# Kernel tuning notes

Measured on AMD Instinct MI355X. Metric: run time of the kernel, lower is better.

## Reference

```python
import jax, jax.numpy as jnp
import numpy as np

N, E, DIN, D, H, L = 4096, 65536, 128, 256, 4, 3
DH = D // H


def _ln(x, g, b, eps=1e-5):
    m = jnp.mean(x, axis=-1, keepdims=True)
    v = jnp.mean((x - m) ** 2, axis=-1, keepdims=True)
    return (x - m) * jax.lax.rsqrt(v + eps) * g + b


def _gcn(x, w, b, row, col, n):
    # PyG GCNConv: add self-loops, symmetric normalization D^-1/2 A D^-1/2, aggregate at col (target)
    ar = jnp.arange(n, dtype=row.dtype)
    r = jnp.concatenate([row, ar])
    c = jnp.concatenate([col, ar])
    deg = jax.ops.segment_sum(jnp.ones(r.shape[0], x.dtype), c, num_segments=n)
    dinv = jnp.where(deg > 0, deg ** -0.5, 0.0)
    norm = dinv[r] * dinv[c]  # (E+N,)
    msg = x @ w.T  # (N, out)
    return jax.ops.segment_sum(norm[:, None] * msg[r], c, num_segments=n) + b


def setup_inputs() -> dict:
    key = jax.random.key(0)
    ks = jax.random.split(key, 12)
    rnd = lambda i, shape: jax.random.normal(ks[i], shape, jnp.float32) * 0.05
    return {
        "node_features": jax.random.normal(ks[0], (N, DIN), jnp.float32),
        "edge_index": jax.random.randint(ks[1], (2, E), 0, N, jnp.int32),
        "gcn1_w": rnd(2, (D, DIN)), "gcn1_b": jnp.zeros((D,), jnp.float32),
        "gcn2_w": rnd(3, (D, D)), "gcn2_b": jnp.zeros((D,), jnp.float32),
        "edge_w": rnd(4, (H, 3)), "edge_b": jnp.zeros((H,), jnp.float32),
        "proj_w": rnd(5, (D, DIN + D)), "proj_b": jnp.zeros((D,), jnp.float32),
        "wqkv": rnd(6, (L, 3 * D, D)), "bqkv": jnp.zeros((L, 3 * D), jnp.float32),
        "wo": rnd(7, (L, D, D)), "bo": jnp.zeros((L, D), jnp.float32),
        "ffn_w1": rnd(8, (L, 4 * D, D)), "ffn_b1": jnp.zeros((L, 4 * D), jnp.float32),
        "ffn_w2": rnd(9, (L, D, 4 * D)), "ffn_b2": jnp.zeros((L, D), jnp.float32),
        "ln1_g": jnp.ones((L, D), jnp.float32), "ln1_b": jnp.zeros((L, D), jnp.float32),
        "ln2_g": jnp.ones((L, D), jnp.float32), "ln2_b": jnp.zeros((L, D), jnp.float32),
        "out_w": rnd(10, (1, D)), "out_b": jnp.zeros((1,), jnp.float32),
    }


def reference(node_features, edge_index, gcn1_w, gcn1_b, gcn2_w, gcn2_b,
              edge_w, edge_b, proj_w, proj_b, wqkv, bqkv, wo, bo,
              ffn_w1, ffn_b1, ffn_w2, ffn_b2, ln1_g, ln1_b, ln2_g, ln2_b,
              out_w, out_b):
    n = node_features.shape[0]
    row, col = edge_index[0], edge_index[1]
    # two-layer GCN
    h = jax.nn.relu(_gcn(node_features, gcn1_w, gcn1_b, row, col, n))
    g = _gcn(h, gcn2_w, gcn2_b, row, col, n)
    x = jnp.concatenate([node_features, g], axis=-1) @ proj_w.T + proj_b  # (N, D)
    # edge-aware attention bias: per-edge linear+sigmoid scattered into dense (H, N, N)
    feat = jnp.stack([row.astype(x.dtype), col.astype(x.dtype),
                      jnp.ones(row.shape[0], x.dtype)], axis=-1)  # (E, 3)
    bpe = jax.nn.sigmoid(feat @ edge_w.T + edge_b)  # (E, H)
    bias = jnp.zeros((H, n, n), x.dtype).at[:, row, col].set(bpe.T)
    scale = 1.0 / np.sqrt(DH)
    for l in range(L):
        qkv = x @ wqkv[l].T + bqkv[l]
        q, k, v = jnp.split(qkv, 3, axis=-1)
        q = q.reshape(n, H, DH); k = k.reshape(n, H, DH); v = v.reshape(n, H, DH)
        s = jnp.einsum('nhd,mhd->hnm', q, k) * scale + bias
        a = jax.nn.softmax(s, axis=-1)
        o = jnp.einsum('hnm,mhd->nhd', a, v).reshape(n, D) @ wo[l].T + bo[l]
        x = _ln(x + o, ln1_g[l], ln1_b[l])
        f = jax.nn.relu(x @ ffn_w1[l].T + ffn_b1[l]) @ ffn_w2[l].T + ffn_b2[l]
        x = _ln(x + f, ln2_g[l], ln2_b[l])
    return jax.nn.sigmoid(x @ out_w.T + out_b)  # (N, 1) probs
```

## Files before the change

kernel.cpp:

```cpp
#include <hip/hip_runtime.h>
#include <math.h>

#define NN 4096
#define NE 65536
#define DIN 128
#define DM 256
#define NH 4
#define NL 3
#define NCH 4
#define TPC (NN / 64 / NCH)
#define NBKT 16384

typedef __attribute__((ext_vector_type(8))) short bf16x8;
typedef __attribute__((ext_vector_type(4))) float f32x4;

__device__ inline ushort f2b(float f) {
    union { float f; uint u; } v; v.f = f;
    uint r = v.u + 0x7fffu + ((v.u >> 16) & 1u);
    return (ushort)(r >> 16);
}

__device__ inline uint cvt_pk_bf16(float lo, float hi) {
    uint r;
    asm("v_cvt_pk_bf16_f32 %0, %1, %2" : "=v"(r) : "v"(lo), "v"(hi));
    return r;
}

__device__ inline void gl_lds16(const ushort* g, ushort* l) {
    __builtin_amdgcn_global_load_lds(
        (const __attribute__((address_space(1))) void*)g,
        (__attribute__((address_space(3))) void*)l, 16, 0, 0);
}


__global__ void k_edge1(const int* __restrict__ row, const int* __restrict__ col,
                        uint* __restrict__ bitmap, int* __restrict__ cnt_c,
                        int* __restrict__ bcnt, unsigned char* __restrict__ flag) {
    int e = blockIdx.x * 256 + threadIdx.x;
    if (e >= NE) return;
    int r = row[e], c = col[e];
    atomicAdd(&cnt_c[c], 1);
    uint idx = (uint)r * 4096u + (uint)c;
    uint m = 1u << (idx & 31);
    uint old = atomicOr(&bitmap[idx >> 5], m);
    int isnew = (old & m) ? 0 : 1;
    flag[e] = (unsigned char)isnew;
    if (isnew) atomicAdd(&bcnt[(r >> 4) * 64 + (c >> 6)], 1);
}

__global__ void k_edge2(const int* __restrict__ row, const int* __restrict__ col,
                        const unsigned char* __restrict__ flag,
                        const int* __restrict__ sc, int* __restrict__ fc, int* __restrict__ csc_row,
                        const int* __restrict__ bstart, int* __restrict__ bfill,
                        ushort* __restrict__ ents) {
    int e = blockIdx.x * 256 + threadIdx.x;
    if (e >= NE) return;
    int r = row[e], c = col[e];
    csc_row[sc[c] + atomicAdd(&fc[c], 1)] = r;
    if (flag[e]) {
        int key = (r >> 4) * 64 + (c >> 6);
        ents[bstart[key] + atomicAdd(&bfill[key], 1)] = (ushort)(((r & 15) << 6) | (c & 63));
    }
}

template <int N>
__global__ void k_scan(const int* __restrict__ cnt, int* __restrict__ start) {
    __shared__ int part[256];
    const int C = N / 256;
    int t = threadIdx.x;
    int s = 0;
    for (int i = 0; i < C; ++i) s += cnt[t * C + i];
    part[t] = s;
    __syncthreads();
    if (t == 0) {
        int acc = 0;
        for (int i = 0; i < 256; ++i) { int v = part[i]; part[i] = acc; acc += v; }
        start[N] = acc;
    }
    __syncthreads();
    int acc = part[t];
    for (int i = 0; i < C; ++i) { start[t * C + i] = acc; acc += cnt[t * C + i]; }
}

__global__ void k_dinv(const int* __restrict__ cnt_c, float* __restrict__ dinv) {
    int i = blockIdx.x * 256 + threadIdx.x;
    if (i < NN) dinv[i] = 1.0f / sqrtf((float)(cnt_c[i] + 1));
}

struct CvtP { const float* s[8]; ushort* d[8]; int n[8]; };
__global__ void k_cvt(CvtP p) {
    int y = blockIdx.y;
    int base = (blockIdx.x * 256 + threadIdx.x) * 4;
    if (base >= p.n[y]) return;
    float4 v = *(const float4*)(p.s[y] + base);
    float sc = 1.f;
    if (y == 1 && ((base >> 8) % 768) < 256) sc = 0.125f;
    ushort4 o;
    o.x = f2b(v.x * sc); o.y = f2b(v.y * sc); o.z = f2b(v.z * sc); o.w = f2b(v.w * sc);
    *(ushort4*)(p.d[y] + base) = o;
}

__global__ void k_scaleb(const float* __restrict__ b, float* __restrict__ o) {
    int i = blockIdx.x * 256 + threadIdx.x;
    if (i < NL * 768) o[i] = b[i] * (((i % 768) < 256) ? 0.125f : 1.f);
}

template <int FLAGS>
__global__ __launch_bounds__(256) void k_gemm_b(
    const ushort* __restrict__ A, int lda,
    const ushort* __restrict__ B, int ldb,
    float* __restrict__ Cf, ushort* __restrict__ Cb, ushort* __restrict__ Cb2, int ldc,
    int K, const float* __restrict__ bias) {
    __shared__ ushort As[128 * 64];
    __shared__ ushort Bs[128 * 64];
    const int tid = threadIdx.x;
    const int w = tid >> 6, l = tid & 63;
    const int l15 = l & 15, l4 = l >> 4;
    const int row0 = blockIdx.y * 128, col0 = blockIdx.x * 128;
    const int wm = (w >> 1) * 64, wn = (w & 1) * 64;
    f32x4 acc[4][4];
#pragma unroll
    for (int i = 0; i < 4; ++i)
#pragma unroll
        for (int j = 0; j < 4; ++j) acc[i][j] = (f32x4){0.f, 0.f, 0.f, 0.f};
    for (int k0 = 0; k0 < K; k0 += 64) {
#pragma unroll
        for (int i = 0; i < 4; ++i) {
            int ci = tid + 256 * i;
            int r = ci >> 3, s = ci & 7;
            bf16x8 va = *(const bf16x8*)(A + (long)(row0 + r) * lda + k0 + s * 8);
            *(bf16x8*)&As[r * 64 + ((s ^ (r & 7)) * 8)] = va;
            bf16x8 vb = *(const bf16x8*)(B + (long)(col0 + r) * ldb + k0 + s * 8);
            *(bf16x8*)&Bs[r * 64 + ((s ^ (r & 7)) * 8)] = vb;
        }
        __syncthreads();
#pragma unroll
        for (int kk = 0; kk < 2; ++kk) {
            bf16x8 af[4], bfr[4];
#pragma unroll
            for (int i = 0; i < 4; ++i) {
                int ar = wm + i * 16 + l15;
                af[i] = *(const bf16x8*)&As[ar * 64 + (((kk * 4 + l4) ^ (ar & 7)) * 8)];
                int br = wn + i * 16 + l15;
                bfr[i] = *(const bf16x8*)&Bs[br * 64 + (((kk * 4 + l4) ^ (br & 7)) * 8)];
            }
#pragma unroll
            for (int i = 0; i < 4; ++i)
#pragma unroll
                for (int j = 0; j < 4; ++j)
                    acc[i][j] = __builtin_amdgcn_mfma_f32_16x16x32_bf16(af[i], bfr[j], acc[i][j], 0, 0, 0);
        }
        __syncthreads();
    }
#pragma unroll
    for (int i = 0; i < 4; ++i)
#pragma unroll
        for (int j = 0; j < 4; ++j) {
            int rb = row0 + wm + i * 16;
            int cb = col0 + wn + j * 16 + l15;
            float bv = bias ? bias[cb] : 0.f;
            if (FLAGS & 16) {
                if (cb < 512) {
#pragma unroll
                    for (int q = 0; q < 4; ++q)
                        Cb[(long)(rb + l4 * 4 + q) * 512 + cb] = f2b(acc[i][j][q] + bv);
                } else {
                    ushort4 o4;
                    o4.x = f2b(acc[i][j][0] + bv);
                    o4.y = f2b(acc[i][j][1] + bv);
                    o4.z = f2b(acc[i][j][2] + bv);
                    o4.w = f2b(acc[i][j][3] + bv);
                    *(ushort4*)(Cb2 + (long)(cb - 512) * NN + rb + l4 * 4) = o4;
                }
            } else if (FLAGS & 8) {
                ushort4 o4;
                o4.x = f2b(acc[i][j][0] + bv);
                o4.y = f2b(acc[i][j][1] + bv);
                o4.z = f2b(acc[i][j][2] + bv);
                o4.w = f2b(acc[i][j][3] + bv);
                *(ushort4*)(Cb + (long)cb * ldc + rb + l4 * 4) = o4;
            } else {
#pragma unroll
                for (int q = 0; q < 4; ++q) {
                    int r = rb + l4 * 4 + q;
                    float v = acc[i][j][q] + bv;
                    if (FLAGS & 4) v = fmaxf(v, 0.f);
                    if (FLAGS & 1) Cf[(long)r * ldc + cb] = v;
                    if (FLAGS & 2) Cb[(long)r * ldc + cb] = f2b(v);
                }
            }
        }
}

__global__ __launch_bounds__(256) void k_gemm_ln(
    const ushort* __restrict__ A, int lda,
    const ushort* __restrict__ B, int ldb, int K,
    const float* __restrict__ bias,
    float* __restrict__ x, ushort* __restrict__ xb,
    const float* __restrict__ gam, const float* __restrict__ bet) {
    __shared__ ushort As[16 * 64];
    __shared__ ushort Bs[256 * 64];
    __shared__ float red[4][16][2];
    const int tid = threadIdx.x;
    const int w = tid >> 6, l = tid & 63;
    const int l15 = l & 15, l4 = l >> 4;
    const int row0 = blockIdx.x * 16;
    f32x4 acc[4];
#pragma unroll
    for (int j = 0; j < 4; ++j) acc[j] = (f32x4){0.f, 0.f, 0.f, 0.f};
    for (int k0 = 0; k0 < K; k0 += 64) {
        if (tid < 128) {
            int r = tid >> 3, s = tid & 7;
            bf16x8 va = *(const bf16x8*)(A + (long)(row0 + r) * lda + k0 + s * 8);
            *(bf16x8*)&As[r * 64 + ((s ^ (r & 7)) * 8)] = va;
        }
#pragma unroll
        for (int i = 0; i < 8; ++i) {
            int idx = i * 256 + tid;
            int r = idx >> 3, s = idx & 7;
            bf16x8 vb = *(const bf16x8*)(B + (long)r * ldb + k0 + s * 8);
            *(bf16x8*)&Bs[r * 64 + ((s ^ (r & 7)) * 8)] = vb;
        }
        __syncthreads();
#pragma unroll
        for (int kk = 0; kk < 2; ++kk) {
            bf16x8 af = *(const bf16x8*)&As[l15 * 64 + (((kk * 4 + l4) ^ (l15 & 7)) * 8)];
#pragma unroll
            for (int j = 0; j < 4; ++j) {
                int br = w * 64 + j * 16 + l15;
                bf16x8 bfr = *(const bf16x8*)&Bs[br * 64 + (((kk * 4 + l4) ^ (br & 7)) * 8)];
                acc[j] = __builtin_amdgcn_mfma_f32_16x16x32_bf16(af, bfr, acc[j], 0, 0, 0);
            }
        }
        __syncthreads();
    }
    float val[4][4];
#pragma unroll
    for (int j = 0; j < 4; ++j) {
        int c = w * 64 + j * 16 + l15;
        float bv = bias[c];
#pragma unroll
        for (int q = 0; q < 4; ++q) {
            int r = row0 + l4 * 4 + q;
            val[j][q] = acc[j][q] + bv + x[(long)r * DM + c];
        }
    }
    float sum[4], sq[4];
#pragma unroll
    for (int q = 0; q < 4; ++q) {
        sum[q] = (val[0][q] + val[1][q]) + (val[2][q] + val[3][q]);
        sq[q] = (val[0][q] * val[0][q] + val[1][q] * val[1][q]) +
                (val[2][q] * val[2][q] + val[3][q] * val[3][q]);
    }
#pragma unroll
    for (int o = 1; o < 16; o <<= 1)
#pragma unroll
        for (int q = 0; q < 4; ++q) {
            sum[q] += __shfl_xor(sum[q], o);
            sq[q] += __shfl_xor(sq[q], o);
        }
    if (l15 == 0)
#pragma unroll
        for (int q = 0; q < 4; ++q) {
            red[w][l4 * 4 + q][0] = sum[q];
            red[w][l4 * 4 + q][1] = sq[q];
        }
    __syncthreads();
    float mean[4], rs[4];
#pragma unroll
    for (int q = 0; q < 4; ++q) {
        int rl = l4 * 4 + q;
        float ts = (red[0][rl][0] + red[1][rl][0]) + (red[2][rl][0] + red[3][rl][0]);
        float tq = (red[0][rl][1] + red[1][rl][1]) + (red[2][rl][1] + red[3][rl][1]);
        float m = ts * (1.f / 256.f);
        float var = tq * (1.f / 256.f) - m * m;
        mean[q] = m;
        rs[q] = rsqrtf(var + 1e-5f);
    }
#pragma unroll
    for (int j = 0; j < 4; ++j) {
        int c = w * 64 + j * 16 + l15;
        float gv = gam[c], bv = bet[c];
#pragma unroll
        for (int q = 0; q < 4; ++q) {
            int r = row0 + l4 * 4 + q;
            float ov = (val[j][q] - mean[q]) * rs[q] * gv + bv;
            x[(long)r * DM + c] = ov;
            xb[(long)r * DM + c] = f2b(ov);
        }
    }
}

template <int ACT, int B16>
__global__ void k_gcn_agg(const float* __restrict__ msg, const int* __restrict__ sc,
                          const int* __restrict__ csc_row, const float* __restrict__ dinv,
                          const float* __restrict__ bias,
                          float* __restrict__ outf, ushort* __restrict__ outb) {
    int j = blockIdx.x;
    int d = threadIdx.x;
    float acc = 0.f;
    int a = sc[j], b = sc[j + 1];
    for (int i = a; i < b; ++i) {
        int r = csc_row[i];
        acc += dinv[r] * msg[(long)r * DM + d];
    }
    float dj = dinv[j];
    float v = dj * acc + dj * dj * msg[(long)j * DM + d] + bias[d];
    if (ACT) v = fmaxf(v, 0.f);
    if (B16) outb[(long)j * DM + d] = f2b(v);
    else outf[(long)j * DM + d] = v;
}

__global__ void k_concat(const ushort* __restrict__ nfb, const float* __restrict__ g,
                         ushort* __restrict__ xcb) {
    long i = (long)blockIdx.x * 256 + threadIdx.x;
    if (i >= (long)NN * 384) return;
    int r = (int)(i / 384), c = (int)(i % 384);
    xcb[i] = (c < DIN) ? nfb[(long)r * DIN + c] : f2b(g[(long)r * DM + (c - DIN)]);
}

__global__ __launch_bounds__(256, 4) void k_attn(
    const ushort* __restrict__ qkb, const ushort* __restrict__ vT,
    const float* __restrict__ ew, const float* __restrict__ eb,
    const int* __restrict__ bstart, const ushort* __restrict__ ents,
    float* __restrict__ opart, float2* __restrict__ ml) {
    __shared__ ushort Klds[2][4096];
    __shared__ ushort Vlds[2][4096];
    __shared__ ushort Pl[4096];
    const int qb = blockIdx.x, h = blockIdx.y, cz = blockIdx.z;
    const int tid = threadIdx.x, w = tid >> 6, l = tid & 63;
    const int l15 = l & 15, l4 = l >> 4;
    const float w0 = ew[h * 3 + 0], w1 = ew[h * 3 + 1], w2 = ew[h * 3 + 2] + eb[h];
    bf16x8 qf[2];
    {
        const ushort* qp = qkb + (long)(qb * 64 + w * 16 + l15) * 512 + h * 64 + l4 * 8;
        qf[0] = *(const bf16x8*)(qp);
        qf[1] = *(const bf16x8*)(qp + 32);
    }
    const ushort* Kb = qkb + 256 + h * 64;
    const ushort* Vb = vT + (long)(h * 64) * NN;
    f32x4 o[4];
#pragma unroll
    for (int f = 0; f < 4; ++f) o[f] = (f32x4){0.f, 0.f, 0.f, 0.f};
    float m_run = -1e30f, l_run = 0.f;
    char* P = (char*)&Pl[w * 1024];
    const int bktW = (qb * 4 + w) * 64;
    const int t0 = cz * TPC;

    auto stage = [&](int b, int t) {
#pragma unroll
        for (int i = 0; i < 2; ++i) {
            int idx = i * 256 + w * 64 + l;
            int r = idx >> 3, sl = idx & 7;
            gl_lds16(Kb + (long)(t * 64 + r) * 512 + ((sl ^ (r & 7)) * 8),
                     &Klds[b][(i * 256 + w * 64) * 8]);
            gl_lds16(Vb + (long)r * NN + t * 64 + ((sl ^ (r & 7)) * 8),
                     &Vlds[b][(i * 256 + w * 64) * 8]);
        }
    };

    int bs_c = bstart[bktW + t0], be_c = bstart[bktW + t0 + 1];
    stage(0, t0);
    int cur = 0;
    for (int tt = 0; tt < TPC; ++tt) {
        const int t = t0 + tt;
        asm volatile("s_waitcnt lgkmcnt(0)" ::: "memory");
        __builtin_amdgcn_s_barrier();
        int bs_n = 0, be_n = 0;
        if (tt + 1 < TPC) {
            stage(cur ^ 1, t + 1);
            bs_n = bstart[bktW + t + 1];
            be_n = bstart[bktW + t + 2];
            asm volatile("s_waitcnt vmcnt(4)" ::: "memory");
        } else {
            asm volatile("s_waitcnt vmcnt(0)" ::: "memory");
        }
        __builtin_amdgcn_sched_barrier(0);
        __builtin_amdgcn_s_barrier();
        __builtin_amdgcn_sched_barrier(0);

        const ushort* Kl = Klds[cur];
        const ushort* Vl = Vlds[cur];
        f32x4 s4[4];
#pragma unroll
        for (int f = 0; f < 4; ++f) {
            int kc = f * 16 + l15;
            bf16x8 k0 = *(const bf16x8*)&Kl[kc * 64 + ((l4 ^ (kc & 7)) * 8)];
            bf16x8 k1 = *(const bf16x8*)&Kl[kc * 64 + (((4 + l4) ^ (kc & 7)) * 8)];
            f32x4 a = (f32x4){0.f, 0.f, 0.f, 0.f};
            a = __builtin_amdgcn_mfma_f32_16x16x32_bf16(k0, qf[0], a, 0, 0, 0);
            a = __builtin_amdgcn_mfma_f32_16x16x32_bf16(k1, qf[1], a, 0, 0, 0);
            s4[f] = a;
        }
        for (int i = bs_c; i < be_c; ++i) {
            int rc = (int)ents[i];
            int r4 = rc >> 6, c6 = rc & 63;
            if (l15 == r4 && ((c6 >> 2) & 3) == l4) {
                float arg = w0 * (float)(qb * 64 + w * 16 + r4) + w1 * (float)(t * 64 + c6) + w2;
                float sig = 1.f / (1.f + __expf(-arg));
                switch (((c6 >> 4) << 2) | (c6 & 3)) {
                    case 0:  s4[0][0] += sig; break; case 1:  s4[0][1] += sig; break;
                    case 2:  s4[0][2] += sig; break; case 3:  s4[0][3] += sig; break;
                    case 4:  s4[1][0] += sig; break; case 5:  s4[1][1] += sig; break;
                    case 6:  s4[1][2] += sig; break; case 7:  s4[1][3] += sig; break;
                    case 8:  s4[2][0] += sig; break; case 9:  s4[2][1] += sig; break;
                    case 10: s4[2][2] += sig; break; case 11: s4[2][3] += sig; break;
                    case 12: s4[3][0] += sig; break; case 13: s4[3][1] += sig; break;
                    case 14: s4[3][2] += sig; break; case 15: s4[3][3] += sig; break;
                }
            }
        }
        float ma = fmaxf(fmaxf(s4[0][0], s4[0][1]), fmaxf(s4[0][2], s4[0][3]));
        float mb = fmaxf(fmaxf(s4[1][0], s4[1][1]), fmaxf(s4[1][2], s4[1][3]));
        float mc = fmaxf(fmaxf(s4[2][0], s4[2][1]), fmaxf(s4[2][2], s4[2][3]));
        float md = fmaxf(fmaxf(s4[3][0], s4[3][1]), fmaxf(s4[3][2], s4[3][3]));
        float me = fmaxf(fmaxf(ma, mb), fmaxf(mc, md));
        me = fmaxf(me, __shfl_xor(me, 16));
        me = fmaxf(me, __shfl_xor(me, 32));
        if (!__all(me <= m_run + 8.f)) {
            float mn = fmaxf(m_run, me);
            float fac = __expf(m_run - mn);
            m_run = mn;
            l_run *= fac;
#pragma unroll
            for (int f = 0; f < 4; ++f)
#pragma unroll
                for (int r = 0; r < 4; ++r) o[f][r] *= fac;
        }
        float rp[4];
#pragma unroll
        for (int f = 0; f < 4; ++f) {
            float p0 = __expf(s4[f][0] - m_run);
            float p1 = __expf(s4[f][1] - m_run);
            float p2 = __expf(s4[f][2] - m_run);
            float p3 = __expf(s4[f][3] - m_run);
            s4[f][0] = p0; s4[f][1] = p1; s4[f][2] = p2; s4[f][3] = p3;
            rp[f] = (p0 + p1) + (p2 + p3);
        }
        float rsum = (rp[0] + rp[1]) + (rp[2] + rp[3]);
        rsum += __shfl_xor(rsum, 16);
        rsum += __shfl_xor(rsum, 32);
        l_run += rsum;
#pragma unroll
        for (int f = 0; f < 4; ++f)
#pragma unroll
            for (int p = 0; p < 2; ++p) {
                uint u = cvt_pk_bf16(s4[f][2 * p], s4[f][2 * p + 1]);
                int slot = f * 2 + (l4 >> 1);
                int byte = l15 * 128 + ((slot ^ (l15 & 7)) << 4) + (l4 & 1) * 8 + p * 4;
                *(uint*)(P + byte) = u;
            }
        asm volatile("s_waitcnt lgkmcnt(0)" ::: "memory");
        __builtin_amdgcn_sched_barrier(0);
#pragma unroll
        for (int ks = 0; ks < 2; ++ks) {
            bf16x8 pb = *(const bf16x8*)(P + l15 * 128 + (((ks * 4 + l4) ^ (l15 & 7)) << 4));
#pragma unroll
            for (int fd = 0; fd < 4; ++fd) {
                int d = fd * 16 + l15;
                bf16x8 vfr = *(const bf16x8*)&Vl[d * 64 + (((ks * 4 + l4) ^ (d & 7)) * 8)];
                o[fd] = __builtin_amdgcn_mfma_f32_16x16x32_bf16(vfr, pb, o[fd], 0, 0, 0);
            }
        }
        bs_c = bs_n; be_c = be_n;
        cur ^= 1;
    }
    long base = (((long)cz * NH + h) * NN + qb * 64 + w * 16 + l15) * 64;
#pragma unroll
    for (int fd = 0; fd < 4; ++fd)
#pragma unroll
        for (int r = 0; r < 4; ++r)
            opart[base + fd * 16 + l4 * 4 + r] = o[fd][r];
    if (l4 == 0)
        ml[((long)cz * NH + h) * NN + qb * 64 + w * 16 + l15] = make_float2(m_run, l_run);
}

__global__ __launch_bounds__(256) void k_comb(const float* __restrict__ opart,
                                              const float2* __restrict__ ml,
                                              ushort* __restrict__ attnOb) {
    int t = blockIdx.x * 256 + threadIdx.x;
    int d = t & 63;
    int r = (t >> 6) & (NN - 1);
    int h = t >> 18;
    float2 mls[NCH];
    float M = -1e30f;
#pragma unroll
    for (int c = 0; c < NCH; ++c) {
        mls[c] = ml[((long)c * NH + h) * NN + r];
        M = fmaxf(M, mls[c].x);
    }
    float s = 0.f, ov = 0.f;
#pragma unroll
    for (int c = 0; c < NCH; ++c) {
        float e = __expf(mls[c].x - M);
        s += mls[c].y * e;
        ov += opart[(((long)c * NH + h) * NN + r) * 64 + d] * e;
    }
    attnOb[(long)r * DM + h * 64 + d] = f2b(ov / s);
}


__global__ void k_out(const float* __restrict__ x, const float* __restrict__ w,
                      const float* __restrict__ b, float* __restrict__ out) {
    int row = blockIdx.x;
    int lane = threadIdx.x;
    float s = 0.f;
#pragma unroll
    for (int i = 0; i < 4; ++i) s += x[(long)row * DM + lane + 64 * i] * w[lane + 64 * i];
#pragma unroll
    for (int o = 1; o < 64; o <<= 1) s += __shfl_xor(s, o);
    if (lane == 0) out[row] = 1.f / (1.f + expf(-(s + b[0])));
}

__global__ void k_sentinel(float* out, int n) {
    int i = blockIdx.x * 256 + threadIdx.x;
    if (i < n) out[i] = 1.0e9f;
}


extern "C" void kernel_launch(void* const* d_in, const int* in_sizes, int n_in,
                              void* d_out, int out_size, void* d_ws, size_t ws_size,
                              hipStream_t stream) {
    const float* nf = (const float*)d_in[0];
    const int* ei = (const int*)d_in[1];
    const int* erow = ei;
    const int* ecol = ei + NE;
    const float* gcn1_w = (const float*)d_in[2];
    const float* gcn1_b = (const float*)d_in[3];
    const float* gcn2_w = (const float*)d_in[4];
    const float* gcn2_b = (const float*)d_in[5];
    const float* edge_w = (const float*)d_in[6];
    const float* edge_b = (const float*)d_in[7];
    const float* proj_w = (const float*)d_in[8];
    const float* proj_b = (const float*)d_in[9];
    const float* wqkv = (const float*)d_in[10];
    const float* bqkv = (const float*)d_in[11];
    const float* wo = (const float*)d_in[12];
    const float* bo = (const float*)d_in[13];
    const float* ffn_w1 = (const float*)d_in[14];
    const float* ffn_b1 = (const float*)d_in[15];
    const float* ffn_w2 = (const float*)d_in[16];
    const float* ffn_b2 = (const float*)d_in[17];
    const float* ln1_g = (const float*)d_in[18];
    const float* ln1_b = (const float*)d_in[19];
    const float* ln2_g = (const float*)d_in[20];
    const float* ln2_b = (const float*)d_in[21];
    const float* out_w = (const float*)d_in[22];
    const float* out_b = (const float*)d_in[23];
    float* out = (float*)d_out;

    char* wp = (char*)d_ws;
    size_t off = 0;
    auto alloc = [&](size_t bytes) -> void* {
        void* p = wp + off;
        off = (off + bytes + 255) & ~(size_t)255;
        return p;
    };
    char* big = (char*)alloc((size_t)NCH * NH * NN * 64 * 4);
    float* msg = (float*)big;
    float* opart = (float*)big;
    ushort* ffnHb = (ushort*)big;
    float* x = (float*)alloc((size_t)NN * DM * 4);
    ushort* xb = (ushort*)alloc((size_t)NN * DM * 2);
    ushort* xcb = (ushort*)alloc((size_t)NN * 384 * 2);
    ushort* hb = (ushort*)alloc((size_t)NN * DM * 2);
    float* g = (float*)alloc((size_t)NN * DM * 4);
    ushort* qkb = (ushort*)alloc((size_t)NN * 512 * 2);
    ushort* vT = (ushort*)alloc((size_t)DM * NN * 2);
    ushort* attnOb = (ushort*)alloc((size_t)NN * DM * 2);
    float2* ml = (float2*)alloc((size_t)NCH * NH * NN * 8);
    ushort* nfb = (ushort*)alloc((size_t)NN * DIN * 2);
    ushort* wqkvb = (ushort*)alloc((size_t)NL * 768 * DM * 2);
    ushort* wob = (ushort*)alloc((size_t)NL * DM * DM * 2);
    ushort* f1b = (ushort*)alloc((size_t)NL * 1024 * DM * 2);
    ushort* f2bw = (ushort*)alloc((size_t)NL * DM * 1024 * 2);
    ushort* g1b = (ushort*)alloc((size_t)DM * DIN * 2);
    ushort* g2b = (ushort*)alloc((size_t)DM * DM * 2);
    ushort* pjb = (ushort*)alloc((size_t)DM * 384 * 2);
    float* bq2 = (float*)alloc((size_t)NL * 768 * 4);
    uint* bitmap = (uint*)alloc((size_t)NN * NN / 8);
    unsigned char* flag = (unsigned char*)alloc(NE);
    int* cnt_c = (int*)alloc((size_t)NN * 4);
    int* bcnt = (int*)alloc((size_t)NBKT * 4);
    int* sc = (int*)alloc((size_t)(NN + 1) * 4);
    int* bstart = (int*)alloc((size_t)(NBKT + 1) * 4);
    int* fc = (int*)alloc((size_t)NN * 4);
    int* bfill = (int*)alloc((size_t)NBKT * 4);
    int* csc_row = (int*)alloc((size_t)NE * 4);
    ushort* ents = (ushort*)alloc((size_t)NE * 2);
    float* dinv = (float*)alloc((size_t)NN * 4);

    if (off > ws_size) {
        k_sentinel<<<(out_size + 255) / 256, 256, 0, stream>>>(out, out_size);
        return;
    }

    hipMemsetAsync(bitmap, 0, (size_t)NN * NN / 8, stream);
    hipMemsetAsync(cnt_c, 0, NN * 4, stream);
    hipMemsetAsync(bcnt, 0, NBKT * 4, stream);
    hipMemsetAsync(fc, 0, NN * 4, stream);
    hipMemsetAsync(bfill, 0, NBKT * 4, stream);
    k_edge1<<<NE / 256, 256, 0, stream>>>(erow, ecol, bitmap, cnt_c, bcnt, flag);
    k_scan<NN><<<1, 256, 0, stream>>>(cnt_c, sc);
    k_scan<NBKT><<<1, 256, 0, stream>>>(bcnt, bstart);
    k_edge2<<<NE / 256, 256, 0, stream>>>(erow, ecol, flag, sc, fc, csc_row, bstart, bfill, ents);
    k_dinv<<<NN / 256, 256, 0, stream>>>(cnt_c, dinv);

    CvtP cp;
    cp.s[0] = nf;      cp.d[0] = nfb;   cp.n[0] = NN * DIN;
    cp.s[1] = wqkv;    cp.d[1] = wqkvb; cp.n[1] = NL * 768 * DM;
    cp.s[2] = wo;      cp.d[2] = wob;   cp.n[2] = NL * DM * DM;
    cp.s[3] = ffn_w1;  cp.d[3] = f1b;   cp.n[3] = NL * 1024 * DM;
    cp.s[4] = ffn_w2;  cp.d[4] = f2bw;  cp.n[4] = NL * DM * 1024;
    cp.s[5] = gcn1_w;  cp.d[5] = g1b;   cp.n[5] = DM * DIN;
    cp.s[6] = gcn2_w;  cp.d[6] = g2b;   cp.n[6] = DM * DM;
    cp.s[7] = proj_w;  cp.d[7] = pjb;   cp.n[7] = DM * 384;
    k_cvt<<<dim3(768, 8), 256, 0, stream>>>(cp);
    k_scaleb<<<(NL * 768 + 255) / 256, 256, 0, stream>>>(bqkv, bq2);

    k_gemm_b<1><<<dim3(DM / 128, NN / 128), 256, 0, stream>>>(
        nfb, DIN, g1b, DIN, msg, nullptr, nullptr, DM, DIN, nullptr);
    k_gcn_agg<1, 1><<<NN, DM, 0, stream>>>(msg, sc, csc_row, dinv, gcn1_b, nullptr, hb);
    k_gemm_b<1><<<dim3(DM / 128, NN / 128), 256, 0, stream>>>(
        hb, DM, g2b, DM, msg, nullptr, nullptr, DM, DM, nullptr);
    k_gcn_agg<0, 0><<<NN, DM, 0, stream>>>(msg, sc, csc_row, dinv, gcn2_b, g, nullptr);
    k_concat<<<(NN * 384 + 255) / 256, 256, 0, stream>>>(nfb, g, xcb);
    k_gemm_b<3><<<dim3(DM / 128, NN / 128), 256, 0, stream>>>(
        xcb, 384, pjb, 384, x, xb, nullptr, DM, 384, proj_b);

    for (int l = 0; l < NL; ++l) {
        k_gemm_b<18><<<dim3(768 / 128, NN / 128), 256, 0, stream>>>(
            xb, DM, wqkvb + (long)l * 768 * DM, DM, nullptr, qkb, vT, 512, DM,
            bq2 + (long)l * 768);
        k_attn<<<dim3(NN / 64, NH, NCH), 256, 0, stream>>>(
            qkb, vT, edge_w, edge_b, bstart, ents, opart, ml);
        k_comb<<<NN * NH * 64 / 256, 256, 0, stream>>>(opart, ml, attnOb);
        k_gemm_ln<<<NN / 16, 256, 0, stream>>>(
            attnOb, DM, wob + (long)l * DM * DM, DM, DM, bo + (long)l * DM,
            x, xb, ln1_g + (long)l * DM, ln1_b + (long)l * DM);
        k_gemm_b<6><<<dim3(1024 / 128, NN / 128), 256, 0, stream>>>(
            xb, DM, f1b + (long)l * 1024 * DM, DM, nullptr, ffnHb, nullptr, 1024, DM,
            ffn_b1 + (long)l * 1024);
        k_gemm_ln<<<NN / 16, 256, 0, stream>>>(
            ffnHb, 1024, f2bw + (long)l * DM * 1024, 1024, 1024, ffn_b2 + (long)l * DM,
            x, xb, ln2_g + (long)l * DM, ln2_b + (long)l * DM);
    }
    k_out<<<NN, 64, 0, stream>>>(x, out_w, out_b, out);
}
```

Measured before the change: 499.4 us.

## Precompute edge sigmoid biases and load V fragments directly into registers

Per-edge sigmoid bias values are computed once per head during edge bucketing and packed as bf16 alongside the position index, instead of recomputing expf in every attention tile of every layer. The attention kernel drops the V LDS staging buffer and loads V MFMA fragments from global memory straight into registers, lowering LDS footprint and LDS traffic. The bias is now stored with bf16 precision, and direct global V loads may expose latency that LDS prefetching previously hid.

```diff
diff --git a/kernel.cpp b/kernel.cpp
--- a/kernel.cpp
+++ b/kernel.cpp
@@ -52,14 +52,23 @@
                         const unsigned char* __restrict__ flag,
                         const int* __restrict__ sc, int* __restrict__ fc, int* __restrict__ csc_row,
                         const int* __restrict__ bstart, int* __restrict__ bfill,
-                        ushort* __restrict__ ents) {
+                        uint* __restrict__ entcomb,
+                        const float* __restrict__ ew, const float* __restrict__ eb) {
     int e = blockIdx.x * 256 + threadIdx.x;
     if (e >= NE) return;
     int r = row[e], c = col[e];
     csc_row[sc[c] + atomicAdd(&fc[c], 1)] = r;
     if (flag[e]) {
         int key = (r >> 4) * 64 + (c >> 6);
-        ents[bstart[key] + atomicAdd(&bfill[key], 1)] = (ushort)(((r & 15) << 6) | (c & 63));
+        int pos = bstart[key] + atomicAdd(&bfill[key], 1);
+        uint idx = (uint)(((r & 15) << 6) | (c & 63));
+        float fr = (float)r, fc2 = (float)c;
+#pragma unroll
+        for (int h = 0; h < NH; ++h) {
+            float arg = ew[h * 3 + 0] * fr + ew[h * 3 + 1] * fc2 + ew[h * 3 + 2] + eb[h];
+            float sig = 1.f / (1.f + __expf(-arg));
+            entcomb[(long)h * NE + pos] = idx | ((uint)f2b(sig) << 16);
+        }
     }
 }
 
@@ -321,16 +330,13 @@
 
 __global__ __launch_bounds__(256, 4) void k_attn(
     const ushort* __restrict__ qkb, const ushort* __restrict__ vT,
-    const float* __restrict__ ew, const float* __restrict__ eb,
-    const int* __restrict__ bstart, const ushort* __restrict__ ents,
+    const int* __restrict__ bstart, const uint* __restrict__ entcomb,
     float* __restrict__ opart, float2* __restrict__ ml) {
     __shared__ ushort Klds[2][4096];
-    __shared__ ushort Vlds[2][4096];
     __shared__ ushort Pl[4096];
     const int qb = blockIdx.x, h = blockIdx.y, cz = blockIdx.z;
     const int tid = threadIdx.x, w = tid >> 6, l = tid & 63;
     const int l15 = l & 15, l4 = l >> 4;
-    const float w0 = ew[h * 3 + 0], w1 = ew[h * 3 + 1], w2 = ew[h * 3 + 2] + eb[h];
     bf16x8 qf[2];
     {
         const ushort* qp = qkb + (long)(qb * 64 + w * 16 + l15) * 512 + h * 64 + l4 * 8;
@@ -339,6 +345,7 @@
     }
     const ushort* Kb = qkb + 256 + h * 64;
     const ushort* Vb = vT + (long)(h * 64) * NN;
+    const uint* ec = entcomb + (long)h * NE;
     f32x4 o[4];
 #pragma unroll
     for (int f = 0; f < 4; ++f) o[f] = (f32x4){0.f, 0.f, 0.f, 0.f};
@@ -350,12 +357,10 @@
     auto stage = [&](int b, int t) {
 #pragma unroll
         for (int i = 0; i < 2; ++i) {
-            int idx = i * 256 + w * 64 + l;
+            int idx = i * 256 + tid;
             int r = idx >> 3, sl = idx & 7;
             gl_lds16(Kb + (long)(t * 64 + r) * 512 + ((sl ^ (r & 7)) * 8),
-                     &Klds[b][(i * 256 + w * 64) * 8]);
-            gl_lds16(Vb + (long)r * NN + t * 64 + ((sl ^ (r & 7)) * 8),
-                     &Vlds[b][(i * 256 + w * 64) * 8]);
+                     &Klds[b][idx * 8]);
         }
     };
 
@@ -366,21 +371,25 @@
         const int t = t0 + tt;
         asm volatile("s_waitcnt lgkmcnt(0)" ::: "memory");
         __builtin_amdgcn_s_barrier();
-        int bs_n = 0, be_n = 0;
-        if (tt + 1 < TPC) {
-            stage(cur ^ 1, t + 1);
-            bs_n = bstart[bktW + t + 1];
-            be_n = bstart[bktW + t + 2];
-            asm volatile("s_waitcnt vmcnt(4)" ::: "memory");
-        } else {
-            asm volatile("s_waitcnt vmcnt(0)" ::: "memory");
-        }
+        stage(cur ^ 1, (t + 1) & 63);
+        __builtin_amdgcn_sched_barrier(0);
+        asm volatile("s_waitcnt vmcnt(2)" ::: "memory");
         __builtin_amdgcn_sched_barrier(0);
         __builtin_amdgcn_s_barrier();
         __builtin_amdgcn_sched_barrier(0);
-
+        int bs_n = 0, be_n = 0;
+        if (tt + 1 < TPC) {
+            bs_n = bstart[bktW + t + 1];
+            be_n = bstart[bktW + t + 2];
+        }
+        bf16x8 vbuf[4][2];
+#pragma unroll
+        for (int fd = 0; fd < 4; ++fd) {
+            const ushort* vp = Vb + (long)(fd * 16 + l15) * NN + t * 64 + l4 * 8;
+            vbuf[fd][0] = *(const bf16x8*)(vp);
+            vbuf[fd][1] = *(const bf16x8*)(vp + 32);
+        }
         const ushort* Kl = Klds[cur];
-        const ushort* Vl = Vlds[cur];
         f32x4 s4[4];
 #pragma unroll
         for (int f = 0; f < 4; ++f) {
@@ -393,11 +402,12 @@
             s4[f] = a;
         }
         for (int i = bs_c; i < be_c; ++i) {
-            int rc = (int)ents[i];
-            int r4 = rc >> 6, c6 = rc & 63;
+            uint e = ec[i];
+            int r4 = (e >> 6) & 15, c6 = e & 63;
             if (l15 == r4 && ((c6 >> 2) & 3) == l4) {
-                float arg = w0 * (float)(qb * 64 + w * 16 + r4) + w1 * (float)(t * 64 + c6) + w2;
-                float sig = 1.f / (1.f + __expf(-arg));
+                union { uint u; float f; } sv;
+                sv.u = e & 0xFFFF0000u;
+                float sig = sv.f;
                 switch (((c6 >> 4) << 2) | (c6 & 3)) {
                     case 0:  s4[0][0] += sig; break; case 1:  s4[0][1] += sig; break;
                     case 2:  s4[0][2] += sig; break; case 3:  s4[0][3] += sig; break;
@@ -456,15 +466,13 @@
         for (int ks = 0; ks < 2; ++ks) {
             bf16x8 pb = *(const bf16x8*)(P + l15 * 128 + (((ks * 4 + l4) ^ (l15 & 7)) << 4));
 #pragma unroll
-            for (int fd = 0; fd < 4; ++fd) {
-                int d = fd * 16 + l15;
-                bf16x8 vfr = *(const bf16x8*)&Vl[d * 64 + (((ks * 4 + l4) ^ (d & 7)) * 8)];
-                o[fd] = __builtin_amdgcn_mfma_f32_16x16x32_bf16(vfr, pb, o[fd], 0, 0, 0);
-            }
+            for (int fd = 0; fd < 4; ++fd)
+                o[fd] = __builtin_amdgcn_mfma_f32_16x16x32_bf16(vbuf[fd][ks], pb, o[fd], 0, 0, 0);
         }
         bs_c = bs_n; be_c = be_n;
         cur ^= 1;
     }
+    asm volatile("s_waitcnt vmcnt(0)" ::: "memory");
     long base = (((long)cz * NH + h) * NN + qb * 64 + w * 16 + l15) * 64;
 #pragma unroll
     for (int fd = 0; fd < 4; ++fd)
@@ -587,7 +595,7 @@
     int* fc = (int*)alloc((size_t)NN * 4);
     int* bfill = (int*)alloc((size_t)NBKT * 4);
     int* csc_row = (int*)alloc((size_t)NE * 4);
-    ushort* ents = (ushort*)alloc((size_t)NE * 2);
+    uint* entcomb = (uint*)alloc((size_t)NH * NE * 4);
     float* dinv = (float*)alloc((size_t)NN * 4);
 
     if (off > ws_size) {
@@ -603,7 +611,8 @@
     k_edge1<<<NE / 256, 256, 0, stream>>>(erow, ecol, bitmap, cnt_c, bcnt, flag);
     k_scan<NN><<<1, 256, 0, stream>>>(cnt_c, sc);
     k_scan<NBKT><<<1, 256, 0, stream>>>(bcnt, bstart);
-    k_edge2<<<NE / 256, 256, 0, stream>>>(erow, ecol, flag, sc, fc, csc_row, bstart, bfill, ents);
+    k_edge2<<<NE / 256, 256, 0, stream>>>(erow, ecol, flag, sc, fc, csc_row, bstart, bfill,
+                                          entcomb, edge_w, edge_b);
     k_dinv<<<NN / 256, 256, 0, stream>>>(cnt_c, dinv);
 
     CvtP cp;
@@ -633,7 +642,7 @@
             xb, DM, wqkvb + (long)l * 768 * DM, DM, nullptr, qkb, vT, 512, DM,
             bq2 + (long)l * 768);
         k_attn<<<dim3(NN / 64, NH, NCH), 256, 0, stream>>>(
-            qkb, vT, edge_w, edge_b, bstart, ents, opart, ml);
+            qkb, vT, bstart, entcomb, opart, ml);
         k_comb<<<NN * NH * 64 / 256, 256, 0, stream>>>(opart, ml, attnOb);
         k_gemm_ln<<<NN / 16, 256, 0, stream>>>(
             attnOb, DM, wob + (long)l * DM * DM, DM, DM, bo + (long)l * DM,
```

Result: slower. 607.7 us (+21.7%).
